# Kernel optimization log

Measured on AMD Instinct MI355X. Metric: run time of the kernel, lower is better.

## Reference

```python
import jax, jax.numpy as jnp
import numpy as np

B, L, D, H = 4, 512, 256, 128  # batch, seq_len, input_size, hidden_size
NEG = -1e30


def setup_inputs() -> dict:
    key = jax.random.key(0)
    ks = jax.random.split(key, 16)
    init = lambda k, shape, fan_in: (jax.random.normal(k, shape, jnp.float32) / np.sqrt(fan_in).astype(np.float32))
    v = jax.random.normal(ks[0], (B, L, D), jnp.float32)
    lengths = jax.random.randint(ks[1], (B,), L // 2, L + 1).astype(jnp.int32)
    p_mask = (jnp.arange(L)[None, :] < lengths[:, None])  # [B, L] bool
    return {
        "v": v,
        "lengths": lengths,
        "p_mask": p_mask,
        "own_W": init(ks[2], (H, D), D), "own_b": jnp.zeros((H,), jnp.float32),
        "comp_W": init(ks[3], (H, D), D), "comp_b": jnp.zeros((H,), jnp.float32),
        "v_attn": init(ks[4], (H,), H),
        "gate_W": init(ks[5], (2 * D, 2 * D), 2 * D), "gate_b": jnp.zeros((2 * D,), jnp.float32),
        "w_ih_f": init(ks[6], (3 * H, 2 * D), 2 * D), "w_hh_f": init(ks[7], (3 * H, H), H),
        "b_ih_f": jnp.zeros((3 * H,), jnp.float32), "b_hh_f": jnp.zeros((3 * H,), jnp.float32),
        "w_ih_b": init(ks[8], (3 * H, 2 * D), 2 * D), "w_hh_b": init(ks[9], (3 * H, H), H),
        "b_ih_b": jnp.zeros((3 * H,), jnp.float32), "b_hh_b": jnp.zeros((3 * H,), jnp.float32),
    }


def _gru(x, tmask, w_ih, w_hh, b_ih, b_hh, reverse):
    """Single-direction GRU over [B, L, In] with length masking (emulates packing)."""
    Bn, Ln, _ = x.shape
    Hn = w_hh.shape[1]
    xp = jnp.einsum('bli,hi->blh', x, w_ih) + b_ih  # [B, L, 3H] input projections

    def step(h, inputs):
        xpt, m = inputs  # [B, 3H], [B, 1]
        hp = h @ w_hh.T + b_hh
        xr, xz, xn = jnp.split(xpt, 3, axis=-1)
        hr, hz, hn = jnp.split(hp, 3, axis=-1)
        r = jax.nn.sigmoid(xr + hr)
        z = jax.nn.sigmoid(xz + hz)
        n = jnp.tanh(xn + r * hn)
        h_new = (1.0 - z) * n + z * h
        h = jnp.where(m, h_new, h)
        return h, jnp.where(m, h_new, jnp.zeros_like(h_new))

    h0 = jnp.zeros((Bn, Hn), x.dtype)
    xs = (jnp.swapaxes(xp, 0, 1), tmask.T[:, :, None])
    _, outs = jax.lax.scan(step, h0, xs, reverse=reverse)
    return jnp.swapaxes(outs, 0, 1)  # [B, L, H]


def reference(v, lengths, p_mask, own_W, own_b, comp_W, comp_b, v_attn,
              gate_W, gate_b, w_ih_f, w_hh_f, b_ih_f, b_hh_f,
              w_ih_b, w_hh_b, b_ih_b, b_hh_b):
    # Additive (Bahdanau / RNet) self-attention, vectorized over all query positions.
    own = v @ own_W.T + own_b    # [B, L, H] (query term)
    comp = v @ comp_W.T + comp_b  # [B, L, H] (key term)
    # scores[b, q, k] = tanh(own_q + comp_k) . v_attn
    scores = jnp.einsum('bqkh,h->bqk', jnp.tanh(own[:, :, None, :] + comp[:, None, :, :]), v_attn)
    scores = jnp.where(p_mask[:, None, :], scores, NEG)  # mask padded keys
    attn = jax.nn.softmax(scores, axis=2)
    C = jnp.einsum('bqk,bkd->bqd', attn, v)  # attended context
    inp = jnp.concatenate([v, C], axis=-1)   # [B, L, 2D]
    inp = jax.nn.sigmoid(inp @ gate_W.T + gate_b) * inp  # gating
    # Bidirectional GRU encoder (pack_padded emulated via time mask; eval mode, no dropout).
    tmask = (jnp.arange(inp.shape[1])[None, :] < lengths[:, None])
    out_f = _gru(inp, tmask, w_ih_f, w_hh_f, b_ih_f, b_hh_f, reverse=False)
    out_b = _gru(inp, tmask, w_ih_b, w_hh_b, b_ih_b, b_hh_b, reverse=True)
    return jnp.concatenate([out_f, out_b], axis=-1)  # [B, L, 2H]
```

## Files before the change

### kernel.cpp

```cpp
#include <hip/hip_runtime.h>
#include <hip/hip_bf16.h>

#define NEGINF -1e30f

typedef __attribute__((ext_vector_type(8))) short short8;
typedef __attribute__((ext_vector_type(4))) float f32x4;
typedef __attribute__((ext_vector_type(4))) int int4_t;

__device__ __forceinline__ float fast_sigmoid(float x) {
    return __builtin_amdgcn_rcpf(1.f + __expf(-x));
}
__device__ __forceinline__ float fast_tanh(float x) {
    return 1.f - 2.f * __builtin_amdgcn_rcpf(1.f + __expf(2.f * x));
}
__device__ __forceinline__ short f2bf(float f) {
    unsigned u = __float_as_uint(f);
    return (short)((u + 0x7fff + ((u >> 16) & 1)) >> 16);
}
__device__ __forceinline__ float bf2f(short b) {
    return __uint_as_float(((unsigned)(unsigned short)b) << 16);
}

__device__ __forceinline__ void bar_lds() {
    asm volatile("s_waitcnt lgkmcnt(0)\n\ts_barrier" ::: "memory");
}

__global__ __launch_bounds__(256) void gemm_bias(
    const float* __restrict__ A,
    const float* __restrict__ W1, const float* __restrict__ b1, float* __restrict__ out1,
    const float* __restrict__ W2, const float* __restrict__ b2, float* __restrict__ out2,
    const int* __restrict__ lengths,
    int M, int N, int K, int nsplit, int mode) {
    const int m0 = blockIdx.y * 64;
    if ((m0 & 511) >= lengths[m0 >> 9]) return;
    __shared__ __align__(16) short Abh[2][2048];
    __shared__ __align__(16) short Abl[2][2048];
    __shared__ __align__(16) short Bbh[2][2048];
    __shared__ __align__(16) short Bbl[2][2048];
    const int tid = threadIdx.x;
    int bx = blockIdx.x;
    const float* W = W1; const float* bias = b1; float* out = out1;
    int n0;
    if (bx < nsplit) {
        n0 = bx * 64;
    } else {
        W = W2; bias = b2; out = out2;
        n0 = (bx - nsplit) * 64;
    }
    const int wave = tid >> 6;
    const int lane = tid & 63;
    const int mrow = lane & 15;
    const int quad = lane >> 4;
    const int wm = (wave >> 1) * 32;
    const int wn = (wave & 1) * 32;

    const int r_ = tid >> 2;
    const int sg = (tid & 3) * 8;

    f32x4 acc[2][2];
#pragma unroll
    for (int mt = 0; mt < 2; mt++)
#pragma unroll
        for (int nt = 0; nt < 2; nt++) acc[mt][nt] = (f32x4){0.f, 0.f, 0.f, 0.f};

    float4 a0 = *(const float4*)(A + (size_t)(m0 + r_) * K + sg);
    float4 a1 = *(const float4*)(A + (size_t)(m0 + r_) * K + sg + 4);
    float4 w0 = *(const float4*)(W + (size_t)(n0 + r_) * K + sg);
    float4 w1 = *(const float4*)(W + (size_t)(n0 + r_) * K + sg + 4);

    for (int k0 = 0; k0 < K; k0 += 32) {
        const int cur = (k0 >> 5) & 1;
        {
            float av[8] = {a0.x, a0.y, a0.z, a0.w, a1.x, a1.y, a1.z, a1.w};
            float wv[8] = {w0.x, w0.y, w0.z, w0.w, w1.x, w1.y, w1.z, w1.w};
            short8 ah, al, bh, bl;
#pragma unroll
            for (int j = 0; j < 8; j++) {
                short h = f2bf(av[j]); ah[j] = h; al[j] = f2bf(av[j] - bf2f(h));
                short g = f2bf(wv[j]); bh[j] = g; bl[j] = f2bf(wv[j] - bf2f(g));
            }
            *(short8*)&Abh[cur][r_ * 32 + sg] = ah;
            *(short8*)&Abl[cur][r_ * 32 + sg] = al;
            *(short8*)&Bbh[cur][r_ * 32 + sg] = bh;
            *(short8*)&Bbl[cur][r_ * 32 + sg] = bl;
        }
        if (k0 + 32 < K) {
            a0 = *(const float4*)(A + (size_t)(m0 + r_) * K + k0 + 32 + sg);
            a1 = *(const float4*)(A + (size_t)(m0 + r_) * K + k0 + 32 + sg + 4);
            w0 = *(const float4*)(W + (size_t)(n0 + r_) * K + k0 + 32 + sg);
            w1 = *(const float4*)(W + (size_t)(n0 + r_) * K + k0 + 32 + sg + 4);
        }
        bar_lds();
        short8 Ah[2], Al[2], Bh[2], Bl[2];
#pragma unroll
        for (int t = 0; t < 2; t++) {
            int ar = (wm + t * 16 + mrow) * 32 + quad * 8;
            int br = (wn + t * 16 + mrow) * 32 + quad * 8;
            Ah[t] = *(const short8*)&Abh[cur][ar];
            Al[t] = *(const short8*)&Abl[cur][ar];
            Bh[t] = *(const short8*)&Bbh[cur][br];
            Bl[t] = *(const short8*)&Bbl[cur][br];
        }
#pragma unroll
        for (int mt = 0; mt < 2; mt++)
#pragma unroll
            for (int nt = 0; nt < 2; nt++) {
                acc[mt][nt] = __builtin_amdgcn_mfma_f32_16x16x32_bf16(Ah[mt], Bh[nt], acc[mt][nt], 0, 0, 0);
                acc[mt][nt] = __builtin_amdgcn_mfma_f32_16x16x32_bf16(Al[mt], Bh[nt], acc[mt][nt], 0, 0, 0);
                acc[mt][nt] = __builtin_amdgcn_mfma_f32_16x16x32_bf16(Ah[mt], Bl[nt], acc[mt][nt], 0, 0, 0);
            }
        bar_lds();
    }
    float bsv[2];
#pragma unroll
    for (int nt = 0; nt < 2; nt++) bsv[nt] = bias[n0 + wn + nt * 16 + mrow];
#pragma unroll
    for (int mt = 0; mt < 2; mt++)
#pragma unroll
        for (int nt = 0; nt < 2; nt++) {
            int n = n0 + wn + nt * 16 + mrow;
#pragma unroll
            for (int r = 0; r < 4; r++) {
                int m = m0 + wm + mt * 16 + quad * 4 + r;
                float val = acc[mt][nt][r] + bsv[nt];
                if (mode == 1) val = fast_sigmoid(val) * A[(size_t)m * K + n];
                out[(size_t)m * N + n] = val;
            }
        }
}

__global__ __launch_bounds__(512) void attn_kernel(
    const float* __restrict__ v, const int* __restrict__ lengths,
    const float* __restrict__ own, const float* __restrict__ comp,
    const float* __restrict__ v_attn, float* __restrict__ inp) {
    const int L = 512, D = 256, H = 128;
    const int b = blockIdx.x >> 6;
    const int q0 = (blockIdx.x & 63) * 8;
    const int len = lengths[b];
    if (q0 >= len) return;
    const int tid = threadIdx.x;
    const float K2E = 2.8853900817779268f;
    __shared__ __align__(16) float oKT[128 * 8];
    __shared__ float va2s[128];
    __shared__ __align__(16) float scf[512 * 12];
    __shared__ float inv8[8];

    for (int i = tid; i < 1024; i += 512) {
        int qq = i >> 7, hh = i & 127;
        oKT[hh * 8 + qq] = K2E * own[((size_t)(b * L + q0 + qq)) * H + hh];
    }
    if (tid < 128) va2s[tid] = -2.f * v_attn[tid];
    __syncthreads();

    {
        const int k = tid;
        float acc[8];
#pragma unroll
        for (int q = 0; q < 8; q++) acc[q] = 0.f;
        if (k < len) {
            const float* cp = comp + ((size_t)(b * L + k)) * H;
            for (int h = 0; h < 128; h += 4) {
                float4 c4 = *(const float4*)(cp + h);
                const float* cv = (const float*)&c4;
#pragma unroll
                for (int j = 0; j < 4; j++) {
                    float cK = cv[j] * K2E;
                    float va = va2s[h + j];
                    float4 o0 = *(const float4*)&oKT[(h + j) * 8];
                    float4 o1 = *(const float4*)&oKT[(h + j) * 8 + 4];
                    const float* op0 = (const float*)&o0;
                    const float* op1 = (const float*)&o1;
#pragma unroll
                    for (int q = 0; q < 4; q++) {
                        float r = __builtin_amdgcn_rcpf(1.f + exp2f(cK + op0[q]));
                        acc[q] = fmaf(va, r, acc[q]);
                    }
#pragma unroll
                    for (int q = 0; q < 4; q++) {
                        float r = __builtin_amdgcn_rcpf(1.f + exp2f(cK + op1[q]));
                        acc[4 + q] = fmaf(va, r, acc[4 + q]);
                    }
                }
            }
#pragma unroll
            for (int q = 0; q < 8; q++) acc[q] = __expf(acc[q]);
        }
        *(float4*)&scf[k * 12] = *(float4*)&acc[0];
        *(float4*)&scf[k * 12 + 4] = *(float4*)&acc[4];
    }
    __syncthreads();

    {
        int w = tid >> 6, l = tid & 63;
        float s = 0.f;
#pragma unroll
        for (int kk = 0; kk < 8; kk++) s += scf[(l + kk * 64) * 12 + w];
#pragma unroll
        for (int off = 1; off < 64; off <<= 1) s += __shfl_xor(s, off);
        if (l == 0) inv8[w] = __builtin_amdgcn_rcpf(s);
    }
    __syncthreads();

    {
        const int d = tid & 255;
        const int qh = tid >> 8;
        float c0 = 0.f, c1 = 0.f, c2 = 0.f, c3 = 0.f;
        const float* vb = v + ((size_t)b * L) * D + d;
        for (int k = 0; k < L; k += 2) {
            float v0 = vb[(size_t)k * D];
            float v1 = vb[(size_t)(k + 1) * D];
            float4 s0 = *(const float4*)&scf[k * 12 + qh * 4];
            float4 s1 = *(const float4*)&scf[(k + 1) * 12 + qh * 4];
            c0 += s0.x * v0 + s1.x * v1;
            c1 += s0.y * v0 + s1.y * v1;
            c2 += s0.z * v0 + s1.z * v1;
            c3 += s0.w * v0 + s1.w * v1;
        }
        float cc[4] = {c0, c1, c2, c3};
#pragma unroll
        for (int j = 0; j < 4; j++) {
            int q = q0 + qh * 4 + j;
            size_t row = ((size_t)(b * L + q)) * 512;
            inp[row + 256 + d] = cc[j] * inv8[qh * 4 + j];
            inp[row + d] = v[((size_t)(b * L + q)) * D + d];
        }
    }
}

__global__ __launch_bounds__(512, 1) void gru_kernel(
    const float* __restrict__ xp_f, const float* __restrict__ xp_b,
    const float* __restrict__ w_hh_f, const float* __restrict__ w_hh_b,
    const float* __restrict__ b_hh_f, const float* __restrict__ b_hh_b,
    const int* __restrict__ lengths, float* __restrict__ out) {
    const int L = 512, H = 128;
    const int dir = blockIdx.x >> 2;
    const int b = blockIdx.x & 3;
    const float* xp = dir ? xp_b : xp_f;
    const float* w_hh = dir ? w_hh_b : w_hh_f;
    const float* b_hh = dir ? b_hh_b : b_hh_f;
    const int tid = threadIdx.x;
    const int wave = tid >> 6;
    const int lane = tid & 63;
    const int mrow = lane & 15;
    const int quad = lane >> 4;
    const int jj = 16 * wave + lane;

    __shared__ __align__(16) signed char hbufc[2][384];

    int4_t wb[3][2];
    float ws[3];
#pragma unroll
    for (int g = 0; g < 3; g++) {
        int row = g * 128 + 16 * wave + mrow;
        float wv[32];
#pragma unroll
        for (int kt = 0; kt < 2; kt++)
#pragma unroll
            for (int j4 = 0; j4 < 4; j4++) {
                float4 f4 = *(const float4*)(w_hh + (size_t)row * H + kt * 64 + quad * 16 + j4 * 4);
                wv[kt * 16 + j4 * 4 + 0] = f4.x;
                wv[kt * 16 + j4 * 4 + 1] = f4.y;
                wv[kt * 16 + j4 * 4 + 2] = f4.z;
                wv[kt * 16 + j4 * 4 + 3] = f4.w;
            }
        float mx = 0.f;
#pragma unroll
        for (int j = 0; j < 32; j++) mx = fmaxf(mx, fabsf(wv[j]));
        mx = fmaxf(mx, __shfl_xor(mx, 16));
        mx = fmaxf(mx, __shfl_xor(mx, 32));
        mx = fmaxf(mx, 1e-30f);
        float inv_s = 127.f / mx;
        ws[g] = (mx / 127.f) * (1.f / 8192.f);
#pragma unroll
        for (int kt = 0; kt < 2; kt++) {
            int tmp[4] = {0, 0, 0, 0};
#pragma unroll
            for (int j = 0; j < 16; j++) {
                int q = (int)rintf(wv[kt * 16 + j] * inv_s);
                tmp[j >> 2] |= (q & 0xff) << ((j & 3) * 8);
            }
            wb[g][kt] = (int4_t){tmp[0], tmp[1], tmp[2], tmp[3]};
        }
    }
    float br = 0.f, bz = 0.f, bn = 0.f, hcur = 0.f;
    if (lane < 16) {
        br = b_hh[jj];
        bz = b_hh[128 + jj];
        bn = b_hh[256 + jj];
    }

    const int len = lengths[b];
    for (int i = tid; i < (L - len) * 128; i += 512) {
        int tt = len + (i >> 7);
        int kk = i & 127;
        out[((size_t)(b * L + tt)) * 256 + dir * 128 + kk] = 0.f;
    }
    for (int i = tid; i < 768; i += 512) ((signed char*)hbufc)[i] = 0;

    const int nch = (len + 15) >> 4;
    float xr[16], xz[16], xn[16];
    if (lane < 16) {
#pragma unroll
        for (int s = 0; s < 16; s++) {
            if (s < len) {
                int t = dir ? (len - 1 - s) : s;
                size_t base = ((size_t)(b * L + t)) * 384;
                xr[s] = xp[base + jj];
                xz[s] = xp[base + 128 + jj];
                xn[s] = xp[base + 256 + jj];
            }
        }
    }
    __syncthreads();

    const int bbase = ((mrow & 1) ? 192 : 0) + quad * 16;
    int par = 0;

    for (int c = 0; c < nch; c++) {
        const int cnt = min(16, len - c * 16);
        float nxr[16], nxz[16], nxn[16];
        if (lane < 16 && c + 1 < nch) {
#pragma unroll
            for (int s = 0; s < 16; s++) {
                int rr = (c + 1) * 16 + s;
                if (rr < len) {
                    int t = dir ? (len - 1 - rr) : rr;
                    size_t base = ((size_t)(b * L + t)) * 384;
                    nxr[s] = xp[base + jj];
                    nxz[s] = xp[base + 128 + jj];
                    nxn[s] = xp[base + 256 + jj];
                }
            }
        }
#pragma unroll
        for (int s = 0; s < 16; s++) {
            if (s < cnt) {
                int4_t af0 = *(const int4_t*)&hbufc[par][bbase];
                int4_t af1 = *(const int4_t*)&hbufc[par][bbase + 64];
                int4_t a0 = (int4_t){0, 0, 0, 0};
                int4_t a1 = (int4_t){0, 0, 0, 0};
                int4_t a2 = (int4_t){0, 0, 0, 0};
                a0 = __builtin_amdgcn_mfma_i32_16x16x64_i8(af0, wb[0][0], a0, 0, 0, 0);
                a0 = __builtin_amdgcn_mfma_i32_16x16x64_i8(af1, wb[0][1], a0, 0, 0, 0);
                a1 = __builtin_amdgcn_mfma_i32_16x16x64_i8(af0, wb[1][0], a1, 0, 0, 0);
                a1 = __builtin_amdgcn_mfma_i32_16x16x64_i8(af1, wb[1][1], a1, 0, 0, 0);
                a2 = __builtin_amdgcn_mfma_i32_16x16x64_i8(af0, wb[2][0], a2, 0, 0, 0);
                a2 = __builtin_amdgcn_mfma_i32_16x16x64_i8(af1, wb[2][1], a2, 0, 0, 0);
                if (lane < 16) {
                    float r = fast_sigmoid(fmaf((float)(a0[0] * 64 + a0[1]), ws[0], xr[s] + br));
                    float z = fast_sigmoid(fmaf((float)(a1[0] * 64 + a1[1]), ws[1], xz[s] + bz));
                    float hh = fmaf((float)(a2[0] * 64 + a2[1]), ws[2], bn);
                    float n = fast_tanh(xn[s] + r * hh);
                    float hn = (1.f - z) * n + z * hcur;
                    hcur = hn;
                    float hs = fminf(fmaxf(hn * 8192.f, -8191.f), 8191.f);
                    int h13 = (int)rintf(hs);
                    int hi = h13 >> 6;
                    int lo = h13 - (hi << 6);
                    hbufc[par ^ 1][jj] = (signed char)hi;
                    hbufc[par ^ 1][192 + jj] = (signed char)lo;
                    int t = dir ? (len - 1 - (c * 16 + s)) : (c * 16 + s);
                    out[((size_t)(b * L + t)) * 256 + dir * 128 + jj] = hn;
                }
                par ^= 1;
                bar_lds();
            }
        }
        if (lane < 16 && c + 1 < nch) {
#pragma unroll
            for (int s = 0; s < 16; s++) { xr[s] = nxr[s]; xz[s] = nxz[s]; xn[s] = nxn[s]; }
        }
    }
}

extern "C" void kernel_launch(void* const* d_in, const int* in_sizes, int n_in,
                              void* d_out, int out_size, void* d_ws, size_t ws_size,
                              hipStream_t stream) {
    const int B = 4, L = 512, D = 256, H = 128;
    const int M = B * L;

    const float* v      = (const float*)d_in[0];
    const int* lengths  = (const int*)d_in[1];
    const float* own_W  = (const float*)d_in[3];
    const float* own_b  = (const float*)d_in[4];
    const float* comp_W = (const float*)d_in[5];
    const float* comp_b = (const float*)d_in[6];
    const float* v_attn = (const float*)d_in[7];
    const float* gate_W = (const float*)d_in[8];
    const float* gate_b = (const float*)d_in[9];
    const float* w_ih_f = (const float*)d_in[10];
    const float* w_hh_f = (const float*)d_in[11];
    const float* b_ih_f = (const float*)d_in[12];
    const float* b_hh_f = (const float*)d_in[13];
    const float* w_ih_b = (const float*)d_in[14];
    const float* w_hh_b = (const float*)d_in[15];
    const float* b_ih_b = (const float*)d_in[16];
    const float* b_hh_b = (const float*)d_in[17];

    float* ws   = (float*)d_ws;
    float* own  = ws;
    float* comp = own + (size_t)M * H;
    float* inp  = comp + (size_t)M * H;
    float* gated = inp + (size_t)M * 512;
    float* xp_f = gated + (size_t)M * 512;
    float* xp_b = xp_f + (size_t)M * 384;
    float* out  = (float*)d_out;

    gemm_bias<<<dim3(4, M / 64), 256, 0, stream>>>(
        v, own_W, own_b, own, comp_W, comp_b, comp, lengths, M, H, D, 2, 0);
    attn_kernel<<<dim3(B * 64), 512, 0, stream>>>(v, lengths, own, comp, v_attn, inp);
    gemm_bias<<<dim3(8, M / 64), 256, 0, stream>>>(
        inp, gate_W, gate_b, gated, gate_W, gate_b, gated, lengths, M, 512, 512, 8, 1);
    gemm_bias<<<dim3(12, M / 64), 256, 0, stream>>>(
        gated, w_ih_f, b_ih_f, xp_f, w_ih_b, b_ih_b, xp_b, lengths, M, 384, 512, 6, 0);
    gru_kernel<<<dim3(8), 512, 0, stream>>>(xp_f, xp_b, w_hh_f, w_hh_b, b_hh_f, b_hh_b, lengths, out);
}
```

Before: 355.4 us.

## Halve GRU workgroup to 4 waves, each computing 32 hidden units per step

```diff
diff --git a/kernel.cpp b/kernel.cpp
--- a/kernel.cpp
+++ b/kernel.cpp
@@ -227,12 +227,15 @@
     }
 }
 
-__global__ __launch_bounds__(512, 1) void gru_kernel(
+__global__ __launch_bounds__(256, 1) void gru_kernel(
     const float* __restrict__ xp_f, const float* __restrict__ xp_b,
     const float* __restrict__ w_hh_f, const float* __restrict__ w_hh_b,
     const float* __restrict__ b_hh_f, const float* __restrict__ b_hh_b,
     const int* __restrict__ lengths, float* __restrict__ out) {
     const int L = 512, H = 128;
+    const float LOG2E = 1.4426950408889634f;
+    const float TWO_LOG2E = 2.8853900817779268f;
+    const int MAGIC_I = 0x4B400000;
     const int dir = blockIdx.x >> 2;
     const int b = blockIdx.x & 3;
     const float* xp = dir ? xp_b : xp_f;
@@ -243,132 +246,165 @@
     const int lane = tid & 63;
     const int mrow = lane & 15;
     const int quad = lane >> 4;
-    const int jj = 16 * wave + lane;
+    const int pos = quad & 1;
+    const int dim = 32 * wave + (lane & 31);
 
     __shared__ __align__(16) signed char hbufc[2][384];
 
-    int4_t wb[3][2];
-    float ws[3];
-#pragma unroll
-    for (int g = 0; g < 3; g++) {
-        int row = g * 128 + 16 * wave + mrow;
-        float wv[32];
-#pragma unroll
-        for (int kt = 0; kt < 2; kt++)
-#pragma unroll
-            for (int j4 = 0; j4 < 4; j4++) {
-                float4 f4 = *(const float4*)(w_hh + (size_t)row * H + kt * 64 + quad * 16 + j4 * 4);
-                wv[kt * 16 + j4 * 4 + 0] = f4.x;
-                wv[kt * 16 + j4 * 4 + 1] = f4.y;
-                wv[kt * 16 + j4 * 4 + 2] = f4.z;
-                wv[kt * 16 + j4 * 4 + 3] = f4.w;
-            }
-        float mx = 0.f;
-#pragma unroll
-        for (int j = 0; j < 32; j++) mx = fmaxf(mx, fabsf(wv[j]));
-        mx = fmaxf(mx, __shfl_xor(mx, 16));
-        mx = fmaxf(mx, __shfl_xor(mx, 32));
-        mx = fmaxf(mx, 1e-30f);
-        float inv_s = 127.f / mx;
-        ws[g] = (mx / 127.f) * (1.f / 8192.f);
-#pragma unroll
-        for (int kt = 0; kt < 2; kt++) {
-            int tmp[4] = {0, 0, 0, 0};
-#pragma unroll
-            for (int j = 0; j < 16; j++) {
-                int q = (int)rintf(wv[kt * 16 + j] * inv_s);
-                tmp[j >> 2] |= (q & 0xff) << ((j & 3) * 8);
-            }
-            wb[g][kt] = (int4_t){tmp[0], tmp[1], tmp[2], tmp[3]};
-        }
-    }
-    float br = 0.f, bz = 0.f, bn = 0.f, hcur = 0.f;
-    if (lane < 16) {
-        br = b_hh[jj];
-        bz = b_hh[128 + jj];
-        bn = b_hh[256 + jj];
-    }
+    int4_t wb[3][2][2];
+    float wsc0, wsc1, wsc2;
+    {
+        float wsl[3][2];
+#pragma unroll
+        for (int g = 0; g < 3; g++) {
+#pragma unroll
+            for (int p = 0; p < 2; p++) {
+                int row = g * 128 + 32 * wave + 16 * p + mrow;
+                float wv[32];
+#pragma unroll
+                for (int kt = 0; kt < 2; kt++)
+#pragma unroll
+                    for (int j4 = 0; j4 < 4; j4++) {
+                        float4 f4 = *(const float4*)(w_hh + (size_t)row * H + kt * 64 + quad * 16 + j4 * 4);
+                        wv[kt * 16 + j4 * 4 + 0] = f4.x;
+                        wv[kt * 16 + j4 * 4 + 1] = f4.y;
+                        wv[kt * 16 + j4 * 4 + 2] = f4.z;
+                        wv[kt * 16 + j4 * 4 + 3] = f4.w;
+                    }
+                float mx = 0.f;
+#pragma unroll
+                for (int j = 0; j < 32; j++) mx = fmaxf(mx, fabsf(wv[j]));
+                mx = fmaxf(mx, __shfl_xor(mx, 16));
+                mx = fmaxf(mx, __shfl_xor(mx, 32));
+                mx = fmaxf(mx, 1e-30f);
+                float inv_s = 127.f / mx;
+                wsl[g][p] = (mx / 127.f) * (1.f / 8192.f);
+#pragma unroll
+                for (int kt = 0; kt < 2; kt++) {
+                    int tmp[4] = {0, 0, 0, 0};
+#pragma unroll
+                    for (int j = 0; j < 16; j++) {
+                        int q = (int)rintf(wv[kt * 16 + j] * inv_s);
+                        tmp[j >> 2] |= (q & 0xff) << ((j & 3) * 8);
+                    }
+                    wb[g][p][kt] = (int4_t){tmp[0], tmp[1], tmp[2], tmp[3]};
+                }
+            }
+        }
+        float s0 = pos ? wsl[0][1] : wsl[0][0];
+        float s1 = pos ? wsl[1][1] : wsl[1][0];
+        float s2 = pos ? wsl[2][1] : wsl[2][0];
+        wsc0 = -s0 * LOG2E;
+        wsc1 = -s1 * LOG2E;
+        wsc2 = s2 * TWO_LOG2E;
+    }
+    const float brl = -b_hh[dim] * LOG2E;
+    const float bzl = -b_hh[128 + dim] * LOG2E;
+    const float bnc = b_hh[256 + dim] * TWO_LOG2E;
+    float hcur = 0.f;
 
     const int len = lengths[b];
-    for (int i = tid; i < (L - len) * 128; i += 512) {
+    for (int i = tid; i < (L - len) * 128; i += 256) {
         int tt = len + (i >> 7);
         int kk = i & 127;
         out[((size_t)(b * L + tt)) * 256 + dir * 128 + kk] = 0.f;
     }
-    for (int i = tid; i < 768; i += 512) ((signed char*)hbufc)[i] = 0;
-
-    const int nch = (len + 15) >> 4;
-    float xr[16], xz[16], xn[16];
-    if (lane < 16) {
-#pragma unroll
-        for (int s = 0; s < 16; s++) {
+    for (int i = tid; i < 768; i += 256) ((signed char*)hbufc)[i] = 0;
+
+    const int CH = 8;
+    const int nch = (len + CH - 1) / CH;
+    float xr[CH], xz[CH], xn[CH];
+    if (lane < 32) {
+#pragma unroll
+        for (int s = 0; s < CH; s++) {
             if (s < len) {
                 int t = dir ? (len - 1 - s) : s;
                 size_t base = ((size_t)(b * L + t)) * 384;
-                xr[s] = xp[base + jj];
-                xz[s] = xp[base + 128 + jj];
-                xn[s] = xp[base + 256 + jj];
+                xr[s] = fmaf(xp[base + dim], -LOG2E, brl);
+                xz[s] = fmaf(xp[base + 128 + dim], -LOG2E, bzl);
+                xn[s] = xp[base + 256 + dim] * TWO_LOG2E;
             }
         }
     }
     __syncthreads();
 
     const int bbase = ((mrow & 1) ? 192 : 0) + quad * 16;
+    const int4_t zero4 = (int4_t){0, 0, 0, 0};
     int par = 0;
 
     for (int c = 0; c < nch; c++) {
-        const int cnt = min(16, len - c * 16);
-        float nxr[16], nxz[16], nxn[16];
-        if (lane < 16 && c + 1 < nch) {
-#pragma unroll
-            for (int s = 0; s < 16; s++) {
-                int rr = (c + 1) * 16 + s;
+        const int cnt = min(CH, len - c * CH);
+        float nxr[CH], nxz[CH], nxn[CH];
+        if (lane < 32 && c + 1 < nch) {
+#pragma unroll
+            for (int s = 0; s < CH; s++) {
+                int rr = (c + 1) * CH + s;
                 if (rr < len) {
                     int t = dir ? (len - 1 - rr) : rr;
                     size_t base = ((size_t)(b * L + t)) * 384;
-                    nxr[s] = xp[base + jj];
-                    nxz[s] = xp[base + 128 + jj];
-                    nxn[s] = xp[base + 256 + jj];
+                    nxr[s] = fmaf(xp[base + dim], -LOG2E, brl);
+                    nxz[s] = fmaf(xp[base + 128 + dim], -LOG2E, bzl);
+                    nxn[s] = xp[base + 256 + dim] * TWO_LOG2E;
                 }
             }
         }
-#pragma unroll
-        for (int s = 0; s < 16; s++) {
+        float hsv[CH];
+#pragma unroll
+        for (int s = 0; s < CH; s++) {
             if (s < cnt) {
                 int4_t af0 = *(const int4_t*)&hbufc[par][bbase];
                 int4_t af1 = *(const int4_t*)&hbufc[par][bbase + 64];
-                int4_t a0 = (int4_t){0, 0, 0, 0};
-                int4_t a1 = (int4_t){0, 0, 0, 0};
-                int4_t a2 = (int4_t){0, 0, 0, 0};
-                a0 = __builtin_amdgcn_mfma_i32_16x16x64_i8(af0, wb[0][0], a0, 0, 0, 0);
-                a0 = __builtin_amdgcn_mfma_i32_16x16x64_i8(af1, wb[0][1], a0, 0, 0, 0);
-                a1 = __builtin_amdgcn_mfma_i32_16x16x64_i8(af0, wb[1][0], a1, 0, 0, 0);
-                a1 = __builtin_amdgcn_mfma_i32_16x16x64_i8(af1, wb[1][1], a1, 0, 0, 0);
-                a2 = __builtin_amdgcn_mfma_i32_16x16x64_i8(af0, wb[2][0], a2, 0, 0, 0);
-                a2 = __builtin_amdgcn_mfma_i32_16x16x64_i8(af1, wb[2][1], a2, 0, 0, 0);
-                if (lane < 16) {
-                    float r = fast_sigmoid(fmaf((float)(a0[0] * 64 + a0[1]), ws[0], xr[s] + br));
-                    float z = fast_sigmoid(fmaf((float)(a1[0] * 64 + a1[1]), ws[1], xz[s] + bz));
-                    float hh = fmaf((float)(a2[0] * 64 + a2[1]), ws[2], bn);
-                    float n = fast_tanh(xn[s] + r * hh);
-                    float hn = (1.f - z) * n + z * hcur;
-                    hcur = hn;
-                    float hs = fminf(fmaxf(hn * 8192.f, -8191.f), 8191.f);
-                    int h13 = (int)rintf(hs);
-                    int hi = h13 >> 6;
-                    int lo = h13 - (hi << 6);
-                    hbufc[par ^ 1][jj] = (signed char)hi;
-                    hbufc[par ^ 1][192 + jj] = (signed char)lo;
-                    int t = dir ? (len - 1 - (c * 16 + s)) : (c * 16 + s);
-                    out[((size_t)(b * L + t)) * 256 + dir * 128 + jj] = hn;
+                int4_t arA = __builtin_amdgcn_mfma_i32_16x16x64_i8(af0, wb[0][0][0], zero4, 0, 0, 0);
+                arA = __builtin_amdgcn_mfma_i32_16x16x64_i8(af1, wb[0][0][1], arA, 0, 0, 0);
+                int4_t arB = __builtin_amdgcn_mfma_i32_16x16x64_i8(af0, wb[0][1][0], zero4, 0, 0, 0);
+                arB = __builtin_amdgcn_mfma_i32_16x16x64_i8(af1, wb[0][1][1], arB, 0, 0, 0);
+                int4_t azA = __builtin_amdgcn_mfma_i32_16x16x64_i8(af0, wb[1][0][0], zero4, 0, 0, 0);
+                azA = __builtin_amdgcn_mfma_i32_16x16x64_i8(af1, wb[1][0][1], azA, 0, 0, 0);
+                int4_t azB = __builtin_amdgcn_mfma_i32_16x16x64_i8(af0, wb[1][1][0], zero4, 0, 0, 0);
+                azB = __builtin_amdgcn_mfma_i32_16x16x64_i8(af1, wb[1][1][1], azB, 0, 0, 0);
+                int4_t anA = __builtin_amdgcn_mfma_i32_16x16x64_i8(af0, wb[2][0][0], zero4, 0, 0, 0);
+                anA = __builtin_amdgcn_mfma_i32_16x16x64_i8(af1, wb[2][0][1], anA, 0, 0, 0);
+                int4_t anB = __builtin_amdgcn_mfma_i32_16x16x64_i8(af0, wb[2][1][0], zero4, 0, 0, 0);
+                anB = __builtin_amdgcn_mfma_i32_16x16x64_i8(af1, wb[2][1][1], anB, 0, 0, 0);
+                int r0 = pos ? arB[0] : arA[0];
+                int r1 = pos ? arB[1] : arA[1];
+                int z0 = pos ? azB[0] : azA[0];
+                int z1 = pos ? azB[1] : azA[1];
+                int n0 = pos ? anB[0] : anA[0];
+                int n1 = pos ? anB[1] : anA[1];
+                float drf = (float)((r0 << 6) + r1);
+                float dzf = (float)((z0 << 6) + z1);
+                float dnf = (float)((n0 << 6) + n1);
+                float r = __builtin_amdgcn_rcpf(1.f + exp2f(fmaf(drf, wsc0, xr[s])));
+                float z = __builtin_amdgcn_rcpf(1.f + exp2f(fmaf(dzf, wsc1, xz[s])));
+                float hh = fmaf(dnf, wsc2, bnc);
+                float n = fmaf(-2.f, __builtin_amdgcn_rcpf(1.f + exp2f(fmaf(r, hh, xn[s]))), 1.f);
+                float hn = fmaf(z, hcur - n, n);
+                hcur = hn;
+                int bi = __float_as_int(fmaf(hn, 8192.f, 12582912.f));
+                bi = min(max(bi, MAGIC_I - 8191), MAGIC_I + 8191);
+                if (lane < 32) {
+                    hbufc[par ^ 1][dim] = (signed char)(bi >> 6);
+                    hbufc[par ^ 1][192 + dim] = (signed char)(bi & 63);
                 }
+                hsv[s] = hn;
                 par ^= 1;
                 bar_lds();
             }
         }
-        if (lane < 16 && c + 1 < nch) {
-#pragma unroll
-            for (int s = 0; s < 16; s++) { xr[s] = nxr[s]; xz[s] = nxz[s]; xn[s] = nxn[s]; }
+        if (lane < 32) {
+#pragma unroll
+            for (int s = 0; s < CH; s++) {
+                if (s < cnt) {
+                    int step = c * CH + s;
+                    int t = dir ? (len - 1 - step) : step;
+                    out[((size_t)(b * L + t)) * 256 + dir * 128 + dim] = hsv[s];
+                }
+            }
+        }
+        if (lane < 32 && c + 1 < nch) {
+#pragma unroll
+            for (int s = 0; s < CH; s++) { xr[s] = nxr[s]; xz[s] = nxz[s]; xn[s] = nxn[s]; }
         }
     }
 }
@@ -413,5 +449,5 @@
         inp, gate_W, gate_b, gated, gate_W, gate_b, gated, lengths, M, 512, 512, 8, 1);
     gemm_bias<<<dim3(12, M / 64), 256, 0, stream>>>(
         gated, w_ih_f, b_ih_f, xp_f, w_ih_b, b_ih_b, xp_b, lengths, M, 384, 512, 6, 0);
-    gru_kernel<<<dim3(8), 512, 0, stream>>>(xp_f, xp_b, w_hh_f, w_hh_b, b_hh_f, b_hh_b, lengths, out);
-}
+    gru_kernel<<<dim3(8), 256, 0, stream>>>(xp_f, xp_b, w_hh_f, w_hh_b, b_hh_f, b_hh_b, lengths, out);
+}
```

Measured after the change: 444.0 us. 1.25x slower.
